# Kernel tuning notes

Measured on AMD Instinct MI355X. Metric: run time of the kernel, lower is better.

## Reference

```python
import jax, jax.numpy as jnp
import numpy as np

H = W = 56
WS = 7          # window size
SHIFT = 3
HEADS = 16
EPS = 1e-5
# padding per SwinMLPBlock: [P_l, P_r, P_t, P_b] = [WS-SHIFT, SHIFT, WS-SHIFT, SHIFT]
P_L, P_R, P_T, P_B = WS - SHIFT, SHIFT, WS - SHIFT, SHIFT


def layer_norm(x, g, b):
    mu = jnp.mean(x, axis=-1, keepdims=True)
    var = jnp.mean(jnp.square(x - mu), axis=-1, keepdims=True)
    return (x - mu) * jax.lax.rsqrt(var + EPS) * g + b


def setup_inputs() -> dict:
    key = jax.random.key(0)
    ks = jax.random.split(key, 8)
    B, L, C = 32, H * W, 512
    hid = 4 * C
    s = lambda fan: 1.0 / np.sqrt(fan)
    return {
        "x": jax.random.normal(ks[0], (B, L, C), jnp.float32),
        "norm1_g": jnp.ones((C,), jnp.float32),
        "norm1_b": jnp.zeros((C,), jnp.float32),
        "spatial_w": jax.random.normal(ks[1], (HEADS, WS * WS, WS * WS), jnp.float32) * s(WS * WS),
        "spatial_b": jax.random.normal(ks[2], (HEADS, WS * WS), jnp.float32) * 0.02,
        "norm2_g": jnp.ones((C,), jnp.float32),
        "norm2_b": jnp.zeros((C,), jnp.float32),
        "fc1_w": jax.random.normal(ks[3], (hid, C), jnp.float32) * s(C),
        "fc1_b": jnp.zeros((hid,), jnp.float32),
        "fc2_w": jax.random.normal(ks[4], (C, hid), jnp.float32) * s(hid),
        "fc2_b": jnp.zeros((C,), jnp.float32),
    }


def reference(x, norm1_g, norm1_b, spatial_w, spatial_b, norm2_g, norm2_b,
              fc1_w, fc1_b, fc2_w, fc2_b):
    B, L, C = x.shape
    hc = C // HEADS
    shortcut = x

    xn = layer_norm(x, norm1_g, norm1_b).reshape(B, H, W, C)
    # shift via zero pad (shift_size > 0 path)
    xp = jnp.pad(xn, ((0, 0), (P_T, P_B), (P_L, P_R), (0, 0)))
    _H, _W = H + WS, W + WS  # 63, 63

    # window partition -> (B*nW, WS*WS, HEADS, hc) -> (n, HEADS, WS*WS, hc)
    xw = xp.reshape(B, _H // WS, WS, _W // WS, WS, C)
    xw = xw.transpose(0, 1, 3, 2, 4, 5).reshape(-1, WS * WS, HEADS, hc)
    xh = xw.transpose(0, 2, 1, 3)  # (n, heads, ws2, hc)

    # grouped conv1d(kernel=1, groups=heads) == per-head [ws2, ws2] matmul
    yh = jnp.einsum('hij,nhjc->nhic', spatial_w, xh) + spatial_b[None, :, :, None]

    # back to windows, then window reverse
    yw = yh.transpose(0, 2, 1, 3).reshape(-1, WS, WS, C)
    y = yw.reshape(B, _H // WS, _W // WS, WS, WS, C)
    y = y.transpose(0, 1, 3, 2, 4, 5).reshape(B, _H, _W, C)
    y = y[:, P_T:_H - P_B, P_L:_W - P_R, :].reshape(B, L, C)

    x = shortcut + y
    # channel MLP with residual
    xn2 = layer_norm(x, norm2_g, norm2_b)
    h = jax.nn.gelu(xn2 @ fc1_w.T + fc1_b, approximate=False)
    return x + (h @ fc2_w.T + fc2_b)
```

## Files before the change

### kernel.cpp

```cpp
#include <hip/hip_runtime.h>

#define HH 56
#define WW 56
#define CC 512
#define BB 32
#define LL (HH*WW)
#define MM (BB*LL)
#define HID 2048

typedef __attribute__((ext_vector_type(8))) __bf16 bf16x8;
typedef __attribute__((ext_vector_type(4))) float f32x4;
typedef __attribute__((ext_vector_type(4))) short s16x4;

__device__ __forceinline__ short f2bf(float f) {
    union { float f; unsigned u; } c; c.f = f;
    unsigned r = c.u + 0x7fffu + ((c.u >> 16) & 1u);
    return (short)(r >> 16);
}
__device__ __forceinline__ float bf2f(short s) {
    union { unsigned u; float f; } c; c.u = ((unsigned)(unsigned short)s) << 16;
    return c.f;
}

__device__ __forceinline__ float gelu_fast(float v) {
    float xg = 0.7978845608f * (v + 0.044715f * v * v * v);
    xg = fminf(xg, 15.0f);
    float t = __expf(2.0f * xg);
    return v * (t / (t + 1.0f));
}

__global__ __launch_bounds__(256) void cvt_bf16(const float* __restrict__ in,
                                                short* __restrict__ out, int n) {
    int i = blockIdx.x * 256 + threadIdx.x;
    if (i < n) out[i] = f2bf(in[i]);
}

__global__ __launch_bounds__(256) void ln512(const float* __restrict__ x,
                                             const float* __restrict__ g,
                                             const float* __restrict__ b,
                                             short* __restrict__ out) {
    const int row = blockIdx.x;
    const int t = threadIdx.x;
    const float2 v = ((const float2*)(x + (long)row * 512))[t];
    float s = v.x + v.y;
    float q = v.x * v.x + v.y * v.y;
#pragma unroll
    for (int off = 32; off > 0; off >>= 1) {
        s += __shfl_xor(s, off, 64);
        q += __shfl_xor(q, off, 64);
    }
    __shared__ float red[8];
    const int wv = t >> 6;
    if ((t & 63) == 0) { red[wv] = s; red[4 + wv] = q; }
    __syncthreads();
    s = red[0] + red[1] + red[2] + red[3];
    q = red[4] + red[5] + red[6] + red[7];
    const float mu = s * (1.0f / 512.0f);
    const float rs = rsqrtf(q * (1.0f / 512.0f) - mu * mu + 1e-5f);
    const float2 gv = ((const float2*)g)[t];
    const float2 bv = ((const float2*)b)[t];
    const float y0 = (v.x - mu) * rs * gv.x + bv.x;
    const float y1 = (v.y - mu) * rs * gv.y + bv.y;
    union { short s2[2]; unsigned u; } o;
    o.s2[0] = f2bf(y0); o.s2[1] = f2bf(y1);
    ((unsigned*)out)[(long)row * 256 + t] = o.u;
}

__global__ __launch_bounds__(256) void spatial_mlp(const short* __restrict__ xn,
                                                   const float* __restrict__ x,
                                                   const float* __restrict__ sw,
                                                   const float* __restrict__ sb,
                                                   float* x1) {
    const int head = blockIdx.y;
    const int t = threadIdx.x;
    const int ch = t & 31;
    const int wloc = t >> 5;
    const int win = blockIdx.x * 8 + wloc;
    const int b = win / 81;
    const int rr = win - b * 81;
    const int wi = rr / 9;
    const int wj = rr - wi * 9;
    const int c = head * 32 + ch;

    float xv[49];
#pragma unroll
    for (int j = 0; j < 49; j++) {
        const int pr = wi * 7 + j / 7 - 4;
        const int pc = wj * 7 + j % 7 - 4;
        float v = 0.0f;
        if (pr >= 0 && pr < 56 && pc >= 0 && pc < 56)
            v = bf2f(xn[((long)((b * 56 + pr) * 56 + pc)) * 512 + c]);
        xv[j] = v;
    }

    const float* swh = sw + head * 2401;
    const float* sbh = sb + head * 49;

#pragma unroll 1
    for (int t7 = 0; t7 < 7; t7++) {
        float acc[7];
#pragma unroll
        for (int ii = 0; ii < 7; ii++) acc[ii] = sbh[t7 * 7 + ii];
#pragma unroll
        for (int ii = 0; ii < 7; ii++) {
            const float* swr = swh + (t7 * 7 + ii) * 49;
#pragma unroll
            for (int j = 0; j < 49; j++)
                acc[ii] = fmaf(swr[j], xv[j], acc[ii]);
        }
        const int pr = wi * 7 + t7 - 4;
        if (pr >= 0 && pr < 56) {
#pragma unroll
            for (int ii = 0; ii < 7; ii++) {
                const int pc = wj * 7 + ii - 4;
                if (pc >= 0 && pc < 56) {
                    const long idx = ((long)((b * 56 + pr) * 56 + pc)) * 512 + c;
                    x1[idx] = x[idx] + acc[ii];
                }
            }
        }
    }
}

template <int K, int N, bool GELU>
__global__ __launch_bounds__(256, 3) void gemm128(const short* __restrict__ A,
                                                  const short* __restrict__ Bw,
                                                  const float* __restrict__ bias,
                                                  const float* res,
                                                  void* Cout) {
    __shared__ __attribute__((aligned(16))) short S[24576];
    const int tid = threadIdx.x;
    const int lane = tid & 63;
    const int wid = tid >> 6;
    const int wr = wid >> 1;
    const int wc = wid & 1;
    const int lr = lane & 15;
    const int kg = (lane >> 4) & 3;

    const int gx = gridDim.x;
    const int lin = blockIdx.y * gx + blockIdx.x;
    const int cpx = (gx * gridDim.y) >> 3;
    const int orig = (lin & 7) * cpx + (lin >> 3);
    const long mBase = (long)(orig / gx) * 128;
    const long nBase = (long)(orig % gx) * 128;

    const int sRow = tid >> 2;
    const int sChunk = (tid & 3) ^ ((tid >> 3) & 3);
    const short* aSrc0 = A + (mBase + sRow) * K + sChunk * 8;
    const short* aSrc1 = A + (mBase + 64 + sRow) * K + sChunk * 8;
    const short* bSrc0 = Bw + (nBase + sRow) * K + sChunk * 8;
    const short* bSrc1 = Bw + (nBase + 64 + sRow) * K + sChunk * 8;

    auto stage = [&](int buf, int t) {
        const long k0 = (long)t * 32;
        char* Ad = (char*)S + buf * 8192 + tid * 16;
        char* Bd = (char*)S + 24576 + buf * 8192 + tid * 16;
        __builtin_amdgcn_global_load_lds(
            (const __attribute__((address_space(1))) void*)(aSrc0 + k0),
            (__attribute__((address_space(3))) void*)Ad, 16, 0, 0);
        __builtin_amdgcn_global_load_lds(
            (const __attribute__((address_space(1))) void*)(aSrc1 + k0),
            (__attribute__((address_space(3))) void*)(Ad + 4096), 16, 0, 0);
        __builtin_amdgcn_global_load_lds(
            (const __attribute__((address_space(1))) void*)(bSrc0 + k0),
            (__attribute__((address_space(3))) void*)Bd, 16, 0, 0);
        __builtin_amdgcn_global_load_lds(
            (const __attribute__((address_space(1))) void*)(bSrc1 + k0),
            (__attribute__((address_space(3))) void*)(Bd + 4096), 16, 0, 0);
    };

    const int swzc = kg ^ ((lr >> 1) & 3);
    const int aOff = (wr * 64 + lr) * 64 + swzc * 16;
    const int bOff = (wc * 64 + lr) * 64 + swzc * 16;

    f32x4 acc[4][4] = {};

    stage(0, 0); stage(1, 1);
    asm volatile("s_waitcnt vmcnt(4)" ::: "memory");
    __builtin_amdgcn_s_barrier();

    const int NT = K / 32;
    int cb = 0;
    for (int t = 0; t < NT; ++t) {
        if (t + 2 < NT) {
            const int sb = cb >= 1 ? cb - 1 : 2;
            stage(sb, t + 2);
        }
        const char* Ab = (const char*)S + cb * 8192;
        const char* Bb = (const char*)S + 24576 + cb * 8192;
        bf16x8 af[4], bf[4];
#pragma unroll
        for (int m = 0; m < 4; ++m) af[m] = *(const bf16x8*)(Ab + aOff + m * 1024);
#pragma unroll
        for (int n = 0; n < 4; ++n) bf[n] = *(const bf16x8*)(Bb + bOff + n * 1024);
        asm volatile("s_waitcnt lgkmcnt(0)" ::: "memory");
        __builtin_amdgcn_s_setprio(1);
#pragma unroll
        for (int m = 0; m < 4; ++m)
#pragma unroll
            for (int n = 0; n < 4; ++n)
                acc[m][n] = __builtin_amdgcn_mfma_f32_16x16x32_bf16(bf[n], af[m],
                                                                    acc[m][n], 0, 0, 0);
        __builtin_amdgcn_s_setprio(0);
        if (t + 1 < NT) {
            if (t + 2 < NT) asm volatile("s_waitcnt vmcnt(4)" ::: "memory");
            else            asm volatile("s_waitcnt vmcnt(0)" ::: "memory");
        }
        __builtin_amdgcn_s_barrier();
        cb = cb + 1 == 3 ? 0 : cb + 1;
    }

#pragma unroll
    for (int n = 0; n < 4; ++n) {
        const long col0 = nBase + wc * 64 + n * 16 + kg * 4;
        const f32x4 bv4 = *(const f32x4*)(bias + col0);
#pragma unroll
        for (int m = 0; m < 4; ++m) {
            const long row = mBase + wr * 64 + m * 16 + lr;
            const long idx = row * N + col0;
            if (GELU) {
                s16x4 o;
#pragma unroll
                for (int r = 0; r < 4; ++r)
                    o[r] = f2bf(gelu_fast(acc[m][n][r] + bv4[r]));
                *(s16x4*)((short*)Cout + idx) = o;
            } else {
                const f32x4 rv = *(const f32x4*)(res + idx);
                f32x4 o;
#pragma unroll
                for (int r = 0; r < 4; ++r) o[r] = acc[m][n][r] + bv4[r] + rv[r];
                *(f32x4*)((float*)Cout + idx) = o;
            }
        }
    }
}

extern "C" void kernel_launch(void* const* d_in, const int* in_sizes, int n_in,
                              void* d_out, int out_size, void* d_ws, size_t ws_size,
                              hipStream_t stream) {
    const float* x    = (const float*)d_in[0];
    const float* n1g  = (const float*)d_in[1];
    const float* n1b  = (const float*)d_in[2];
    const float* sw   = (const float*)d_in[3];
    const float* sb   = (const float*)d_in[4];
    const float* n2g  = (const float*)d_in[5];
    const float* n2b  = (const float*)d_in[6];
    const float* fc1w = (const float*)d_in[7];
    const float* fc1b = (const float*)d_in[8];
    const float* fc2w = (const float*)d_in[9];
    const float* fc2b = (const float*)d_in[10];
    float* out = (float*)d_out;

    char* ws = (char*)d_ws;
    short* xn  = (short*)ws;
    short* hb  = (short*)(ws + 102760448);
    short* w1b = (short*)(ws + 513802240);
    short* w2b = (short*)(ws + 515899392);

    cvt_bf16<<<4096, 256, 0, stream>>>(fc1w, w1b, 2048 * 512);
    cvt_bf16<<<4096, 256, 0, stream>>>(fc2w, w2b, 512 * 2048);

    ln512<<<MM, 256, 0, stream>>>(x, n1g, n1b, xn);

    spatial_mlp<<<dim3(324, 16), 256, 0, stream>>>(xn, x, sw, sb, out);

    ln512<<<MM, 256, 0, stream>>>(out, n2g, n2b, xn);

    gemm128<512, 2048, true><<<dim3(16, 784), 256, 0, stream>>>(xn, w1b, fc1b, nullptr, hb);

    gemm128<2048, 512, false><<<dim3(4, 784), 256, 0, stream>>>(hb, w2b, fc2b, out, out);
}
```

Measured before the change: 1.204 ms.

## Enlarge GEMM tiles to 256x128 with 8 waves and BK=64 split pipeline

Both MLP GEMMs move from 128x128 tiles with 4 waves and K-step 32 to 256x128 tiles with 8 waves and K-step 64. A and B are staged separately into a triple-buffered 144KB LDS layout with an 8-chunk XOR swizzle, and each K-step is split into two MFMA halves so the next A and B loads are issued between them. The intent is more reuse of each staged operand and fewer barriers per unit of work. The cost is a larger LDS footprint, which limits occupancy, and extra barriers inside each step.

```diff
diff --git a/kernel.cpp b/kernel.cpp
--- a/kernel.cpp
+++ b/kernel.cpp
@@ -123,17 +123,17 @@
 }
 
 template <int K, int N, bool GELU>
-__global__ __launch_bounds__(256, 3) void gemm128(const short* __restrict__ A,
+__global__ __launch_bounds__(512, 2) void gemm256(const short* __restrict__ A,
                                                   const short* __restrict__ Bw,
                                                   const float* __restrict__ bias,
                                                   const float* res,
                                                   void* Cout) {
-    __shared__ __attribute__((aligned(16))) short S[24576];
+    __shared__ __attribute__((aligned(16))) short S[73728];
     const int tid = threadIdx.x;
     const int lane = tid & 63;
     const int wid = tid >> 6;
-    const int wr = wid >> 1;
-    const int wc = wid & 1;
+    const int wm = wid >> 1;
+    const int wn = wid & 1;
     const int lr = lane & 15;
     const int kg = (lane >> 4) & 3;
 
@@ -141,58 +141,58 @@
     const int lin = blockIdx.y * gx + blockIdx.x;
     const int cpx = (gx * gridDim.y) >> 3;
     const int orig = (lin & 7) * cpx + (lin >> 3);
-    const long mBase = (long)(orig / gx) * 128;
+    const long mBase = (long)(orig / gx) * 256;
     const long nBase = (long)(orig % gx) * 128;
 
-    const int sRow = tid >> 2;
-    const int sChunk = (tid & 3) ^ ((tid >> 3) & 3);
-    const short* aSrc0 = A + (mBase + sRow) * K + sChunk * 8;
-    const short* aSrc1 = A + (mBase + 64 + sRow) * K + sChunk * 8;
-    const short* bSrc0 = Bw + (nBase + sRow) * K + sChunk * 8;
-    const short* bSrc1 = Bw + (nBase + 64 + sRow) * K + sChunk * 8;
-
-    auto stage = [&](int buf, int t) {
-        const long k0 = (long)t * 32;
-        char* Ad = (char*)S + buf * 8192 + tid * 16;
-        char* Bd = (char*)S + 24576 + buf * 8192 + tid * 16;
-        __builtin_amdgcn_global_load_lds(
-            (const __attribute__((address_space(1))) void*)(aSrc0 + k0),
-            (__attribute__((address_space(3))) void*)Ad, 16, 0, 0);
-        __builtin_amdgcn_global_load_lds(
-            (const __attribute__((address_space(1))) void*)(aSrc1 + k0),
-            (__attribute__((address_space(3))) void*)(Ad + 4096), 16, 0, 0);
-        __builtin_amdgcn_global_load_lds(
-            (const __attribute__((address_space(1))) void*)(bSrc0 + k0),
-            (__attribute__((address_space(3))) void*)Bd, 16, 0, 0);
-        __builtin_amdgcn_global_load_lds(
-            (const __attribute__((address_space(1))) void*)(bSrc1 + k0),
-            (__attribute__((address_space(3))) void*)(Bd + 4096), 16, 0, 0);
+    const int sRow = tid >> 3;
+    const int sChunk = (tid & 7) ^ ((tid >> 3) & 7);
+    const short* aS = A + (mBase + sRow) * K + sChunk * 8;
+    const short* bS = Bw + (nBase + sRow) * K + sChunk * 8;
+
+    auto stageA = [&](int t) {
+        const int r = t % 3;
+        const long k0 = (long)t * 64;
+        char* d = (char*)S + r * 32768 + tid * 16;
+#pragma unroll
+        for (int j = 0; j < 4; ++j)
+            __builtin_amdgcn_global_load_lds(
+                (const __attribute__((address_space(1))) void*)(aS + k0 + (long)j * 64 * K),
+                (__attribute__((address_space(3))) void*)(d + j * 8192), 16, 0, 0);
     };
-
-    const int swzc = kg ^ ((lr >> 1) & 3);
-    const int aOff = (wr * 64 + lr) * 64 + swzc * 16;
-    const int bOff = (wc * 64 + lr) * 64 + swzc * 16;
+    auto stageB = [&](int t) {
+        const int r = t % 3;
+        const long k0 = (long)t * 64;
+        char* d = (char*)S + 98304 + r * 16384 + tid * 16;
+#pragma unroll
+        for (int j = 0; j < 2; ++j)
+            __builtin_amdgcn_global_load_lds(
+                (const __attribute__((address_space(1))) void*)(bS + k0 + (long)j * 64 * K),
+                (__attribute__((address_space(3))) void*)(d + j * 8192), 16, 0, 0);
+    };
+
+    const int c0 = ((0 + kg) ^ (lr & 7)) * 16;
+    const int c1 = ((4 + kg) ^ (lr & 7)) * 16;
+    const int aRow0 = (wm * 64 + lr) * 128;
+    const int bRow0 = (wn * 64 + lr) * 128;
 
     f32x4 acc[4][4] = {};
 
-    stage(0, 0); stage(1, 1);
-    asm volatile("s_waitcnt vmcnt(4)" ::: "memory");
+    stageA(0); stageB(0); stageA(1); stageB(1);
+    asm volatile("s_waitcnt vmcnt(6)" ::: "memory");
     __builtin_amdgcn_s_barrier();
 
-    const int NT = K / 32;
-    int cb = 0;
+    const int NT = K / 64;
     for (int t = 0; t < NT; ++t) {
-        if (t + 2 < NT) {
-            const int sb = cb >= 1 ? cb - 1 : 2;
-            stage(sb, t + 2);
-        }
-        const char* Ab = (const char*)S + cb * 8192;
-        const char* Bb = (const char*)S + 24576 + cb * 8192;
+        const char* Ab = (const char*)S + (t % 3) * 32768;
+        const char* Bb = (const char*)S + 98304 + (t % 3) * 16384;
         bf16x8 af[4], bf[4];
-#pragma unroll
-        for (int m = 0; m < 4; ++m) af[m] = *(const bf16x8*)(Ab + aOff + m * 1024);
-#pragma unroll
-        for (int n = 0; n < 4; ++n) bf[n] = *(const bf16x8*)(Bb + bOff + n * 1024);
+
+#pragma unroll
+        for (int m = 0; m < 4; ++m) af[m] = *(const bf16x8*)(Ab + aRow0 + m * 2048 + c0);
+#pragma unroll
+        for (int n = 0; n < 4; ++n) bf[n] = *(const bf16x8*)(Bb + bRow0 + n * 2048 + c0);
+        if (t + 2 < NT) stageA(t + 2);
+        __builtin_amdgcn_s_barrier();
         asm volatile("s_waitcnt lgkmcnt(0)" ::: "memory");
         __builtin_amdgcn_s_setprio(1);
 #pragma unroll
@@ -202,21 +202,35 @@
                 acc[m][n] = __builtin_amdgcn_mfma_f32_16x16x32_bf16(bf[n], af[m],
                                                                     acc[m][n], 0, 0, 0);
         __builtin_amdgcn_s_setprio(0);
-        if (t + 1 < NT) {
-            if (t + 2 < NT) asm volatile("s_waitcnt vmcnt(4)" ::: "memory");
-            else            asm volatile("s_waitcnt vmcnt(0)" ::: "memory");
-        }
-        __builtin_amdgcn_s_barrier();
-        cb = cb + 1 == 3 ? 0 : cb + 1;
+        __builtin_amdgcn_s_barrier();
+
+#pragma unroll
+        for (int m = 0; m < 4; ++m) af[m] = *(const bf16x8*)(Ab + aRow0 + m * 2048 + c1);
+#pragma unroll
+        for (int n = 0; n < 4; ++n) bf[n] = *(const bf16x8*)(Bb + bRow0 + n * 2048 + c1);
+        if (t + 2 < NT) stageB(t + 2);
+        __builtin_amdgcn_s_barrier();
+        asm volatile("s_waitcnt lgkmcnt(0)" ::: "memory");
+        __builtin_amdgcn_s_setprio(1);
+#pragma unroll
+        for (int m = 0; m < 4; ++m)
+#pragma unroll
+            for (int n = 0; n < 4; ++n)
+                acc[m][n] = __builtin_amdgcn_mfma_f32_16x16x32_bf16(bf[n], af[m],
+                                                                    acc[m][n], 0, 0, 0);
+        __builtin_amdgcn_s_setprio(0);
+        if (t + 2 < NT)      asm volatile("s_waitcnt vmcnt(6)" ::: "memory");
+        else if (t + 1 < NT) asm volatile("s_waitcnt vmcnt(0)" ::: "memory");
+        __builtin_amdgcn_s_barrier();
     }
 
 #pragma unroll
     for (int n = 0; n < 4; ++n) {
-        const long col0 = nBase + wc * 64 + n * 16 + kg * 4;
+        const long col0 = nBase + wn * 64 + n * 16 + kg * 4;
         const f32x4 bv4 = *(const f32x4*)(bias + col0);
 #pragma unroll
         for (int m = 0; m < 4; ++m) {
-            const long row = mBase + wr * 64 + m * 16 + lr;
+            const long row = mBase + wm * 64 + m * 16 + lr;
             const long idx = row * N + col0;
             if (GELU) {
                 s16x4 o;
@@ -266,7 +280,7 @@
 
     ln512<<<MM, 256, 0, stream>>>(out, n2g, n2b, xn);
 
-    gemm128<512, 2048, true><<<dim3(16, 784), 256, 0, stream>>>(xn, w1b, fc1b, nullptr, hb);
-
-    gemm128<2048, 512, false><<<dim3(4, 784), 256, 0, stream>>>(hb, w2b, fc2b, out, out);
-}
+    gemm256<512, 2048, true><<<dim3(16, 392), 512, 0, stream>>>(xn, w1b, fc1b, nullptr, hb);
+
+    gemm256<2048, 512, false><<<dim3(4, 392), 512, 0, stream>>>(hb, w2b, fc2b, out, out);
+}
```

Result: no change. 1.191 ms (-1.1%).
